# Optimization experiments

Measured on AMD Instinct MI355X. Metric: run time of the kernel, lower is better.

Reference implementation:

```python
import jax, jax.numpy as jnp
import numpy as np

B, D_IN, D_H = 16384, 512, 512


def setup_inputs() -> dict:
    key = jax.random.key(0)
    ks = jax.random.split(key, 12)
    scale_w = (2.0 / (D_IN + D_H)) ** 0.5  # xavier-normal-ish
    inp = {
        "X_t": jax.random.normal(ks[0], (B, D_IN), jnp.float32),
        "c_prev": jax.random.normal(ks[1], (B, D_H), jnp.float32),
        "W_f": jax.random.normal(ks[2], (D_IN, D_H), jnp.float32) * scale_w,
        "W_i": jax.random.normal(ks[3], (D_IN, D_H), jnp.float32) * scale_w,
        "W_o": jax.random.normal(ks[4], (D_IN, D_H), jnp.float32) * scale_w,
        "W_c": jax.random.normal(ks[5], (D_IN, D_H), jnp.float32) * scale_w,
        "U_f": jax.random.normal(ks[6], (D_H, D_H), jnp.float32) * (1.0 / D_H ** 0.5),
        "U_i": jax.random.normal(ks[7], (D_H, D_H), jnp.float32) * (1.0 / D_H ** 0.5),
        "U_o": jax.random.normal(ks[8], (D_H, D_H), jnp.float32) * (1.0 / D_H ** 0.5),
        "U_c": jax.random.normal(ks[9], (D_H, D_H), jnp.float32) * (1.0 / D_H ** 0.5),
        "b_f": jnp.zeros((D_H,), jnp.float32),
        "b_i": jnp.zeros((D_H,), jnp.float32),
        "b_o": jnp.zeros((D_H,), jnp.float32),
        "b_c": jnp.zeros((D_H,), jnp.float32),
    }
    return inp


def reference(X_t, c_prev, W_f, W_i, W_o, W_c, U_f, U_i, U_o, U_c, b_f, b_i, b_o, b_c):
    # Fuse the 8 small GEMMs into 2 batched GEMMs (same math: block-concat weights).
    W = jnp.concatenate([W_f, W_i, W_o, W_c], axis=1)  # [D_in, 4H]
    U = jnp.concatenate([U_f, U_i, U_o, U_c], axis=1)  # [H, 4H]
    b = jnp.concatenate([b_f, b_i, b_o, b_c], axis=0)  # [4H]
    pre = X_t @ W + c_prev @ U + b  # [B, 4H]
    f_pre, i_pre, o_pre, c_pre = jnp.split(pre, 4, axis=1)
    f_t = jax.nn.sigmoid(f_pre)
    i_t = jax.nn.sigmoid(i_pre)
    o_t = jax.nn.sigmoid(o_pre)
    c_hat = jnp.tanh(c_pre)
    c_t = f_t * c_prev + i_t * c_hat
    h_t = o_t * jnp.tanh(c_t)
    return h_t
```

## Files before the change

kernel.cpp:

```cpp
#include <hip/hip_runtime.h>

typedef float f32x4 __attribute__((ext_vector_type(4)));
typedef short s16x8 __attribute__((ext_vector_type(8)));
typedef unsigned short u16x8 __attribute__((ext_vector_type(8)));
typedef unsigned int u32;

__device__ __forceinline__ unsigned short f2bf(float f) {
  u32 x = __float_as_uint(f);
  u32 r = (x + 0x7fffu + ((x >> 16) & 1u)) >> 16;
  return (unsigned short)r;
}

__device__ __forceinline__ void gload16(const void* g, void* lds) {
  __builtin_amdgcn_global_load_lds(
      (const __attribute__((address_space(1))) u32*)(uintptr_t)g,
      (__attribute__((address_space(3))) u32*)(u32)(uintptr_t)lds,
      16, 0, 0);
}

__global__ __launch_bounds__(256) void pack_a_kernel(const float* __restrict__ X,
                                                     const float* __restrict__ C,
                                                     unsigned short* __restrict__ At) {
  int idx = blockIdx.x * 256 + threadIdx.x;
  int row = idx >> 7;
  int kc = idx & 127;
  const float* src = (kc < 64) ? (X + row * 512 + kc * 8)
                               : (C + row * 512 + (kc - 64) * 8);
  float4 v0 = *(const float4*)src;
  float4 v1 = *(const float4*)(src + 4);
  u16x8 h;
  h[0] = f2bf(v0.x); h[1] = f2bf(v0.y); h[2] = f2bf(v0.z); h[3] = f2bf(v0.w);
  h[4] = f2bf(v1.x); h[5] = f2bf(v1.y); h[6] = f2bf(v1.z); h[7] = f2bf(v1.w);
  int tile = ((row >> 7) << 4) + (kc >> 3);
  int r = row & 127, c = kc & 7;
  char* dst = (char*)At + (size_t)tile * 16384 + r * 128 + ((c ^ (r & 7)) << 4);
  *(u16x8*)dst = h;
}

__global__ __launch_bounds__(256) void pack_b_kernel(
    const float* __restrict__ Wf, const float* __restrict__ Wi,
    const float* __restrict__ Wo, const float* __restrict__ Wc,
    const float* __restrict__ Uf, const float* __restrict__ Ui,
    const float* __restrict__ Uo, const float* __restrict__ Uc,
    unsigned short* __restrict__ Bt) {
  __shared__ float T[64][68];
  int bid = blockIdx.x;
  int kt = bid & 15;
  int jt = (bid >> 4) & 7;
  int g = bid >> 7;
  const float* Wg = (g == 0) ? Wf : (g == 1) ? Wi : (g == 2) ? Wo : Wc;
  const float* Ug = (g == 0) ? Uf : (g == 1) ? Ui : (g == 2) ? Uo : Uc;
  const float* srcbase = (kt < 8) ? (Wg + (size_t)kt * 64 * 512)
                                  : (Ug + (size_t)(kt - 8) * 64 * 512);
  int j0 = jt * 64;
  int tid = threadIdx.x;
  int kk = tid >> 2, q = tid & 3;
  const float* rp = srcbase + (size_t)kk * 512 + j0 + q * 16;
  float4 a = *(const float4*)(rp);
  float4 b = *(const float4*)(rp + 4);
  float4 c4 = *(const float4*)(rp + 8);
  float4 d = *(const float4*)(rp + 12);
  *(float4*)&T[kk][q * 16] = a;
  *(float4*)&T[kk][q * 16 + 4] = b;
  *(float4*)&T[kk][q * 16 + 8] = c4;
  *(float4*)&T[kk][q * 16 + 12] = d;
  __syncthreads();
  for (int ci = tid; ci < 512; ci += 256) {
    int jj = ci >> 3, c = ci & 7;
    u16x8 h;
#pragma unroll
    for (int e = 0; e < 8; ++e) h[e] = f2bf(T[c * 8 + e][jj]);
    int j = j0 + jj;
    int n = ((j >> 4) << 6) + (g << 4) + (j & 15);
    int NB = n >> 7, r = n & 127;
    char* dst = (char*)Bt + (size_t)(NB * 16 + kt) * 16384 + r * 128 +
                ((c ^ (r & 7)) << 4);
    *(u16x8*)dst = h;
  }
}

__global__ __launch_bounds__(256, 2) void gemm_fused(
    const unsigned short* __restrict__ At, const unsigned short* __restrict__ Bt,
    const float* __restrict__ c_prev,
    const float* __restrict__ bf_, const float* __restrict__ bi_,
    const float* __restrict__ bo_, const float* __restrict__ bc_,
    float* __restrict__ H) {
  __shared__ __align__(16) char As[16384];
  __shared__ __align__(16) char Bs[16384];
  int bid = blockIdx.x;
  int wg = (bid & 7) * 256 + (bid >> 3);
  int bn = wg & 15, bm = wg >> 4;
  int tid = threadIdx.x;
  int lane = tid & 63, w = tid >> 6;
  int wr = w >> 1, wc = w & 1;
  int l15 = lane & 15, kq = lane >> 4;

  const char* gA = (const char*)At + (size_t)bm * (16 * 16384) + w * 4096 + lane * 16;
  const char* gB = (const char*)Bt + (size_t)bn * (16 * 16384) + w * 4096 + lane * 16;

  f32x4 acc[4][4] = {};

  int aoff[4][2], boff[4][2];
#pragma unroll
  for (int m = 0; m < 4; ++m) {
    int r = wr * 64 + m * 16 + l15;
    aoff[m][0] = r * 128 + (((kq) ^ (r & 7)) << 4);
    aoff[m][1] = r * 128 + (((kq + 4) ^ (r & 7)) << 4);
  }
#pragma unroll
  for (int n = 0; n < 4; ++n) {
    int r = wc * 64 + n * 16 + l15;
    boff[n][0] = r * 128 + (((kq) ^ (r & 7)) << 4);
    boff[n][1] = r * 128 + (((kq + 4) ^ (r & 7)) << 4);
  }

  for (int ks = 0; ks < 16; ++ks) {
    __syncthreads();
#pragma unroll
    for (int i = 0; i < 4; ++i) {
      gload16(gA + ks * 16384 + i * 1024, As + w * 4096 + i * 1024);
      gload16(gB + ks * 16384 + i * 1024, Bs + w * 4096 + i * 1024);
    }
    __syncthreads();
    s16x8 a[4][2], b[4][2];
#pragma unroll
    for (int m = 0; m < 4; ++m) {
      a[m][0] = *(const s16x8*)(As + aoff[m][0]);
      a[m][1] = *(const s16x8*)(As + aoff[m][1]);
    }
#pragma unroll
    for (int n = 0; n < 4; ++n) {
      b[n][0] = *(const s16x8*)(Bs + boff[n][0]);
      b[n][1] = *(const s16x8*)(Bs + boff[n][1]);
    }
#pragma unroll
    for (int m = 0; m < 4; ++m)
#pragma unroll
      for (int n = 0; n < 4; ++n) {
        acc[m][n] = __builtin_amdgcn_mfma_f32_16x16x32_bf16(a[m][0], b[n][0], acc[m][n], 0, 0, 0);
        acc[m][n] = __builtin_amdgcn_mfma_f32_16x16x32_bf16(a[m][1], b[n][1], acc[m][n], 0, 0, 0);
      }
  }

  int jgroup = 2 * bn + wc;
  int j = jgroup * 16 + l15;
  float vbf = bf_[j], vbi = bi_[j], vbo = bo_[j], vbc = bc_[j];
  int row0 = bm * 128 + wr * 64 + kq * 4;
#pragma unroll
  for (int m = 0; m < 4; ++m) {
#pragma unroll
    for (int ri = 0; ri < 4; ++ri) {
      int row = row0 + m * 16 + ri;
      float fp = acc[m][0][ri] + vbf;
      float ip = acc[m][1][ri] + vbi;
      float op = acc[m][2][ri] + vbo;
      float cq = acc[m][3][ri] + vbc;
      float ft = 1.0f / (1.0f + __expf(-fp));
      float it = 1.0f / (1.0f + __expf(-ip));
      float ot = 1.0f / (1.0f + __expf(-op));
      float ch = 1.0f - 2.0f / (1.0f + __expf(2.0f * cq));
      float cp = c_prev[(size_t)row * 512 + j];
      float ct = ft * cp + it * ch;
      float th = 1.0f - 2.0f / (1.0f + __expf(2.0f * ct));
      H[(size_t)row * 512 + j] = ot * th;
    }
  }
}

extern "C" void kernel_launch(void* const* d_in, const int* in_sizes, int n_in,
                              void* d_out, int out_size, void* d_ws, size_t ws_size,
                              hipStream_t stream) {
  const float* X = (const float*)d_in[0];
  const float* Cp = (const float*)d_in[1];
  const float* Wf = (const float*)d_in[2];
  const float* Wi = (const float*)d_in[3];
  const float* Wo = (const float*)d_in[4];
  const float* Wc = (const float*)d_in[5];
  const float* Uf = (const float*)d_in[6];
  const float* Ui = (const float*)d_in[7];
  const float* Uo = (const float*)d_in[8];
  const float* Uc = (const float*)d_in[9];
  const float* bfp = (const float*)d_in[10];
  const float* bip = (const float*)d_in[11];
  const float* bop = (const float*)d_in[12];
  const float* bcp = (const float*)d_in[13];
  float* H = (float*)d_out;

  unsigned short* At = (unsigned short*)d_ws;
  unsigned short* Bt = (unsigned short*)((char*)d_ws + 33554432u);

  pack_a_kernel<<<8192, 256, 0, stream>>>(X, Cp, At);
  pack_b_kernel<<<512, 256, 0, stream>>>(Wf, Wi, Wo, Wc, Uf, Ui, Uo, Uc, Bt);
  gemm_fused<<<2048, 256, 0, stream>>>(At, Bt, Cp, bfp, bip, bop, bcp, H);
}
```

Measured before the change: 95.63 us.

## Use 256x256 tiles with 8 waves and a multi-stage pipelined LDS GEMM

```diff
diff --git a/kernel.cpp b/kernel.cpp
--- a/kernel.cpp
+++ b/kernel.cpp
@@ -18,23 +18,26 @@
       16, 0, 0);
 }
 
+
 __global__ __launch_bounds__(256) void pack_a_kernel(const float* __restrict__ X,
                                                      const float* __restrict__ C,
                                                      unsigned short* __restrict__ At) {
   int idx = blockIdx.x * 256 + threadIdx.x;
-  int row = idx >> 7;
-  int kc = idx & 127;
-  const float* src = (kc < 64) ? (X + row * 512 + kc * 8)
-                               : (C + row * 512 + (kc - 64) * 8);
+  int u = idx >> 10;
+  int co = idx & 1023;
+  int r = co >> 2, cl = co & 3;
+  int bm = u >> 5, ks = (u >> 1) & 15, kh = u & 1;
+  int row = bm * 256 + r;
+  int kq = cl ^ ((r >> 1) & 3);
+  int k = ks * 64 + kh * 32 + kq * 8;
+  const float* src = (k < 512) ? (X + (size_t)row * 512 + k)
+                               : (C + (size_t)row * 512 + (k - 512));
   float4 v0 = *(const float4*)src;
   float4 v1 = *(const float4*)(src + 4);
   u16x8 h;
   h[0] = f2bf(v0.x); h[1] = f2bf(v0.y); h[2] = f2bf(v0.z); h[3] = f2bf(v0.w);
   h[4] = f2bf(v1.x); h[5] = f2bf(v1.y); h[6] = f2bf(v1.z); h[7] = f2bf(v1.w);
-  int tile = ((row >> 7) << 4) + (kc >> 3);
-  int r = row & 127, c = kc & 7;
-  char* dst = (char*)At + (size_t)tile * 16384 + r * 128 + ((c ^ (r & 7)) << 4);
-  *(u16x8*)dst = h;
+  *(u16x8*)((char*)At + (size_t)idx * 16) = h;
 }
 
 __global__ __launch_bounds__(256) void pack_b_kernel(
@@ -43,111 +46,126 @@
     const float* __restrict__ Uf, const float* __restrict__ Ui,
     const float* __restrict__ Uo, const float* __restrict__ Uc,
     unsigned short* __restrict__ Bt) {
-  __shared__ float T[64][68];
-  int bid = blockIdx.x;
-  int kt = bid & 15;
-  int jt = (bid >> 4) & 7;
-  int g = bid >> 7;
+  int idx = blockIdx.x * 256 + threadIdx.x;
+  int u = idx >> 10;
+  int co = idx & 1023;
+  int r = co >> 2, cl = co & 3;
+  int bn = u >> 5, ks = (u >> 1) & 15, kh = u & 1;
+  int n = bn * 256 + r;
+  int g = (n >> 4) & 3;
+  int j = ((n >> 6) << 4) | (n & 15);
+  int kq = cl ^ ((r >> 1) & 3);
+  int k = ks * 64 + kh * 32 + kq * 8;
   const float* Wg = (g == 0) ? Wf : (g == 1) ? Wi : (g == 2) ? Wo : Wc;
   const float* Ug = (g == 0) ? Uf : (g == 1) ? Ui : (g == 2) ? Uo : Uc;
-  const float* srcbase = (kt < 8) ? (Wg + (size_t)kt * 64 * 512)
-                                  : (Ug + (size_t)(kt - 8) * 64 * 512);
-  int j0 = jt * 64;
-  int tid = threadIdx.x;
-  int kk = tid >> 2, q = tid & 3;
-  const float* rp = srcbase + (size_t)kk * 512 + j0 + q * 16;
-  float4 a = *(const float4*)(rp);
-  float4 b = *(const float4*)(rp + 4);
-  float4 c4 = *(const float4*)(rp + 8);
-  float4 d = *(const float4*)(rp + 12);
-  *(float4*)&T[kk][q * 16] = a;
-  *(float4*)&T[kk][q * 16 + 4] = b;
-  *(float4*)&T[kk][q * 16 + 8] = c4;
-  *(float4*)&T[kk][q * 16 + 12] = d;
-  __syncthreads();
-  for (int ci = tid; ci < 512; ci += 256) {
-    int jj = ci >> 3, c = ci & 7;
-    u16x8 h;
+  const float* M = (k < 512) ? (Wg + (size_t)k * 512) : (Ug + (size_t)(k - 512) * 512);
+  u16x8 h;
 #pragma unroll
-    for (int e = 0; e < 8; ++e) h[e] = f2bf(T[c * 8 + e][jj]);
-    int j = j0 + jj;
-    int n = ((j >> 4) << 6) + (g << 4) + (j & 15);
-    int NB = n >> 7, r = n & 127;
-    char* dst = (char*)Bt + (size_t)(NB * 16 + kt) * 16384 + r * 128 +
-                ((c ^ (r & 7)) << 4);
-    *(u16x8*)dst = h;
-  }
-}
-
-__global__ __launch_bounds__(256, 2) void gemm_fused(
-    const unsigned short* __restrict__ At, const unsigned short* __restrict__ Bt,
+  for (int e = 0; e < 8; ++e) h[e] = f2bf(M[(size_t)e * 512 + j]);
+  *(u16x8*)((char*)Bt + (size_t)idx * 16) = h;
+}
+
+
+#define BAR    asm volatile("s_barrier" ::: "memory")
+#define WAITV8 asm volatile("s_waitcnt vmcnt(8)" ::: "memory")
+#define LGKM0  do { asm volatile("s_waitcnt lgkmcnt(0)" ::: "memory"); \
+                    __builtin_amdgcn_sched_barrier(0); } while (0)
+
+#define STAGE_A(KS, KH, PDST)                                              \
+  do { const char* s_ = gA + (((KS) * 2 + (KH)) << 14) + tid * 16;         \
+       char* d_ = lds + (((PDST) * 2 + (KH)) << 14) + tid * 16;            \
+       gload16(s_, d_); gload16(s_ + 8192, d_ + 8192); } while (0)
+#define STAGE_B(KS, KH, PDST)                                              \
+  do { const char* s_ = gB + (((KS) * 2 + (KH)) << 14) + tid * 16;         \
+       char* d_ = lds + 65536 + (((PDST) * 2 + (KH)) << 14) + tid * 16;    \
+       gload16(s_, d_); gload16(s_ + 8192, d_ + 8192); } while (0)
+
+#define MFMA1(M, N) acc[M][N] = __builtin_amdgcn_mfma_f32_16x16x32_bf16(a##M##_, b##N##_, acc[M][N], 0, 0, 0)
+
+#define PHASE(PAR, KH, MH, STAGE, WAITSTMT)                                          \
+  do {                                                                               \
+    const char* Ab_ = lds + (((PAR) * 2 + (KH)) << 14) + wr * 8192 + (MH) * 4096;    \
+    const char* Bb_ = lds + 65536 + (((PAR) * 2 + (KH)) << 14) + wc * 4096;          \
+    s16x8 a0_ = *(const s16x8*)(Ab_ + 0 * 1024 + lsw);                               \
+    s16x8 a1_ = *(const s16x8*)(Ab_ + 1 * 1024 + lsw);                               \
+    s16x8 a2_ = *(const s16x8*)(Ab_ + 2 * 1024 + lsw);                               \
+    s16x8 a3_ = *(const s16x8*)(Ab_ + 3 * 1024 + lsw);                               \
+    s16x8 b0_ = *(const s16x8*)(Bb_ + 0 * 1024 + lsw);                               \
+    s16x8 b1_ = *(const s16x8*)(Bb_ + 1 * 1024 + lsw);                               \
+    s16x8 b2_ = *(const s16x8*)(Bb_ + 2 * 1024 + lsw);                               \
+    s16x8 b3_ = *(const s16x8*)(Bb_ + 3 * 1024 + lsw);                               \
+    STAGE;                                                                           \
+    WAITSTMT;                                                                        \
+    BAR;                                                                             \
+    LGKM0;                                                                           \
+    __builtin_amdgcn_s_setprio(1);                                                   \
+    { enum { M0 = (MH) * 4, M1 = M0 + 1, M2 = M0 + 2, M3 = M0 + 3 };                 \
+      acc[M0][0] = __builtin_amdgcn_mfma_f32_16x16x32_bf16(a0_, b0_, acc[M0][0],0,0,0); \
+      acc[M1][0] = __builtin_amdgcn_mfma_f32_16x16x32_bf16(a1_, b0_, acc[M1][0],0,0,0); \
+      acc[M2][0] = __builtin_amdgcn_mfma_f32_16x16x32_bf16(a2_, b0_, acc[M2][0],0,0,0); \
+      acc[M3][0] = __builtin_amdgcn_mfma_f32_16x16x32_bf16(a3_, b0_, acc[M3][0],0,0,0); \
+      acc[M0][1] = __builtin_amdgcn_mfma_f32_16x16x32_bf16(a0_, b1_, acc[M0][1],0,0,0); \
+      acc[M1][1] = __builtin_amdgcn_mfma_f32_16x16x32_bf16(a1_, b1_, acc[M1][1],0,0,0); \
+      acc[M2][1] = __builtin_amdgcn_mfma_f32_16x16x32_bf16(a2_, b1_, acc[M2][1],0,0,0); \
+      acc[M3][1] = __builtin_amdgcn_mfma_f32_16x16x32_bf16(a3_, b1_, acc[M3][1],0,0,0); \
+      acc[M0][2] = __builtin_amdgcn_mfma_f32_16x16x32_bf16(a0_, b2_, acc[M0][2],0,0,0); \
+      acc[M1][2] = __builtin_amdgcn_mfma_f32_16x16x32_bf16(a1_, b2_, acc[M1][2],0,0,0); \
+      acc[M2][2] = __builtin_amdgcn_mfma_f32_16x16x32_bf16(a2_, b2_, acc[M2][2],0,0,0); \
+      acc[M3][2] = __builtin_amdgcn_mfma_f32_16x16x32_bf16(a3_, b2_, acc[M3][2],0,0,0); \
+      acc[M0][3] = __builtin_amdgcn_mfma_f32_16x16x32_bf16(a0_, b3_, acc[M0][3],0,0,0); \
+      acc[M1][3] = __builtin_amdgcn_mfma_f32_16x16x32_bf16(a1_, b3_, acc[M1][3],0,0,0); \
+      acc[M2][3] = __builtin_amdgcn_mfma_f32_16x16x32_bf16(a2_, b3_, acc[M2][3],0,0,0); \
+      acc[M3][3] = __builtin_amdgcn_mfma_f32_16x16x32_bf16(a3_, b3_, acc[M3][3],0,0,0); \
+    }                                                                                \
+    __builtin_amdgcn_s_setprio(0);                                                   \
+    __builtin_amdgcn_sched_barrier(0);                                               \
+    BAR;                                                                             \
+  } while (0)
+
+__global__ __launch_bounds__(512, 2) void gemm_fused(
+    const unsigned short* __restrict__ At_, const unsigned short* __restrict__ Bt_,
     const float* __restrict__ c_prev,
     const float* __restrict__ bf_, const float* __restrict__ bi_,
     const float* __restrict__ bo_, const float* __restrict__ bc_,
     float* __restrict__ H) {
-  __shared__ __align__(16) char As[16384];
-  __shared__ __align__(16) char Bs[16384];
+  __shared__ __attribute__((aligned(128))) char lds[131072];
   int bid = blockIdx.x;
-  int wg = (bid & 7) * 256 + (bid >> 3);
-  int bn = wg & 15, bm = wg >> 4;
+  int wg = (bid & 7) * 64 + (bid >> 3);
+  int bn = wg & 7, bm = wg >> 3;
   int tid = threadIdx.x;
   int lane = tid & 63, w = tid >> 6;
-  int wr = w >> 1, wc = w & 1;
+  int wr = w >> 2, wc = w & 3;
   int l15 = lane & 15, kq = lane >> 4;
-
-  const char* gA = (const char*)At + (size_t)bm * (16 * 16384) + w * 4096 + lane * 16;
-  const char* gB = (const char*)Bt + (size_t)bn * (16 * 16384) + w * 4096 + lane * 16;
-
-  f32x4 acc[4][4] = {};
-
-  int aoff[4][2], boff[4][2];
+  int lsw = l15 * 64 + ((kq ^ ((l15 >> 1) & 3)) << 4);
+
+  const char* gA = (const char*)At_ + (size_t)bm * (32 * 16384);
+  const char* gB = (const char*)Bt_ + (size_t)bn * (32 * 16384);
+
+  f32x4 acc[8][4] = {};
+
+  STAGE_A(0, 0, 0); STAGE_B(0, 0, 0);
+  STAGE_A(0, 1, 0); STAGE_B(0, 1, 0);
+  STAGE_A(1, 0, 1); STAGE_B(1, 0, 1);
+  WAITV8;
+  BAR;
+
+  for (int t = 0; t < 16; t += 2) {
+    int p1 = (t + 1) & 15, p2 = (t + 2) & 15, p3 = (t + 3) & 15;
+    PHASE(0, 0, 0, STAGE_A(p1, 1, 1), );
+    PHASE(0, 0, 1, STAGE_B(p1, 1, 1), WAITV8);
+    PHASE(0, 1, 0, STAGE_A(p2, 0, 0), );
+    PHASE(0, 1, 1, STAGE_B(p2, 0, 0), WAITV8);
+    PHASE(1, 0, 0, STAGE_A(p2, 1, 0), );
+    PHASE(1, 0, 1, STAGE_B(p2, 1, 0), WAITV8);
+    PHASE(1, 1, 0, STAGE_A(p3, 0, 1), );
+    PHASE(1, 1, 1, STAGE_B(p3, 0, 1), WAITV8);
+  }
+
+  int j = (bn * 4 + wc) * 16 + l15;
+  float vbf = bf_[j], vbi = bi_[j], vbo = bo_[j], vbc = bc_[j];
+  int row0 = bm * 256 + wr * 128 + kq * 4;
 #pragma unroll
-  for (int m = 0; m < 4; ++m) {
-    int r = wr * 64 + m * 16 + l15;
-    aoff[m][0] = r * 128 + (((kq) ^ (r & 7)) << 4);
-    aoff[m][1] = r * 128 + (((kq + 4) ^ (r & 7)) << 4);
-  }
-#pragma unroll
-  for (int n = 0; n < 4; ++n) {
-    int r = wc * 64 + n * 16 + l15;
-    boff[n][0] = r * 128 + (((kq) ^ (r & 7)) << 4);
-    boff[n][1] = r * 128 + (((kq + 4) ^ (r & 7)) << 4);
-  }
-
-  for (int ks = 0; ks < 16; ++ks) {
-    __syncthreads();
-#pragma unroll
-    for (int i = 0; i < 4; ++i) {
-      gload16(gA + ks * 16384 + i * 1024, As + w * 4096 + i * 1024);
-      gload16(gB + ks * 16384 + i * 1024, Bs + w * 4096 + i * 1024);
-    }
-    __syncthreads();
-    s16x8 a[4][2], b[4][2];
-#pragma unroll
-    for (int m = 0; m < 4; ++m) {
-      a[m][0] = *(const s16x8*)(As + aoff[m][0]);
-      a[m][1] = *(const s16x8*)(As + aoff[m][1]);
-    }
-#pragma unroll
-    for (int n = 0; n < 4; ++n) {
-      b[n][0] = *(const s16x8*)(Bs + boff[n][0]);
-      b[n][1] = *(const s16x8*)(Bs + boff[n][1]);
-    }
-#pragma unroll
-    for (int m = 0; m < 4; ++m)
-#pragma unroll
-      for (int n = 0; n < 4; ++n) {
-        acc[m][n] = __builtin_amdgcn_mfma_f32_16x16x32_bf16(a[m][0], b[n][0], acc[m][n], 0, 0, 0);
-        acc[m][n] = __builtin_amdgcn_mfma_f32_16x16x32_bf16(a[m][1], b[n][1], acc[m][n], 0, 0, 0);
-      }
-  }
-
-  int jgroup = 2 * bn + wc;
-  int j = jgroup * 16 + l15;
-  float vbf = bf_[j], vbi = bi_[j], vbo = bo_[j], vbc = bc_[j];
-  int row0 = bm * 128 + wr * 64 + kq * 4;
-#pragma unroll
-  for (int m = 0; m < 4; ++m) {
+  for (int m = 0; m < 8; ++m) {
 #pragma unroll
     for (int ri = 0; ri < 4; ++ri) {
       int row = row0 + m * 16 + ri;
@@ -190,6 +208,6 @@
   unsigned short* Bt = (unsigned short*)((char*)d_ws + 33554432u);
 
   pack_a_kernel<<<8192, 256, 0, stream>>>(X, Cp, At);
-  pack_b_kernel<<<512, 256, 0, stream>>>(Wf, Wi, Wo, Wc, Uf, Ui, Uo, Uc, Bt);
-  gemm_fused<<<2048, 256, 0, stream>>>(At, Bt, Cp, bfp, bip, bop, bcp, H);
-}
+  pack_b_kernel<<<1024, 256, 0, stream>>>(Wf, Wi, Wo, Wc, Uf, Ui, Uo, Uc, Bt);
+  gemm_fused<<<512, 512, 0, stream>>>(At, Bt, Cp, bfp, bip, bop, bcp, H);
+}
```

After: 100.1 us. +4.6%, slower.
